# Performance work log

Hardware: AMD Instinct MI355X
Metric: run time of the kernel (lower is better)

Reference implementation:

```python
import math
import jax, jax.numpy as jnp
import numpy as np

MAX_DEGREE = 4
FOUR_PI = 4.0 * math.pi


def _assoc_legendre(ct, st, L):
    """Associated Legendre P_l^m(ct) with Condon-Shortley phase, m>=0.
    Returns dict P[(l, m)] of arrays shaped like ct."""
    P = {(0, 0): jnp.ones_like(ct)}
    # diagonal: P_m^m = (-1)^m (2m-1)!! st^m
    for m in range(1, L + 1):
        P[(m, m)] = (-(2 * m - 1)) * st * P[(m - 1, m - 1)]
    # subdiagonal: P_{m+1}^m = (2m+1) ct P_m^m
    for m in range(0, L):
        P[(m + 1, m)] = (2 * m + 1) * ct * P[(m, m)]
    # recurrence: (l-m) P_l^m = (2l-1) ct P_{l-1}^m - (l+m-1) P_{l-2}^m
    for m in range(0, L + 1):
        for l in range(m + 2, L + 1):
            P[(l, m)] = ((2 * l - 1) * ct * P[(l - 1, m)]
                         - (l + m - 1) * P[(l - 2, m)]) / (l - m)
    return P


def _sph_harm_embed(directions, L=MAX_DEGREE):
    x, y, z = directions[..., 0], directions[..., 1], directions[..., 2]
    ct = jnp.clip(z, -1.0, 1.0)                      # cos(theta)
    st = jnp.sqrt(jnp.clip(1.0 - ct * ct, 0.0, 1.0))  # sin(theta) >= 0
    phi = jnp.arctan2(y, x)
    P = _assoc_legendre(ct, st, L)
    harmonics = []
    for l in range(L + 1):
        for m in range(-l, l + 1):
            am = abs(m)
            N = math.sqrt((2 * l + 1) / FOUR_PI
                          * math.factorial(l - am) / math.factorial(l + am))
            base = N * P[(l, am)]
            re = base * jnp.cos(am * phi)
            im = base * jnp.sin(am * phi)
            if m < 0:  # Y_{l,-m} = (-1)^m conj(Y_{l,m})
                s = (-1.0) ** am
                re, im = s * re, -s * im
            harmonics.append(re)
            harmonics.append(im)
    # matches torch.stack(harmonics, dim=-1): [B, N, 2*(L+1)^2]
    return jnp.stack(harmonics, axis=-1)


def setup_inputs() -> dict:
    key = jax.random.key(0)
    d = jax.random.normal(key, (8, 262144, 3), dtype=jnp.float32)
    d = d / jnp.linalg.norm(d, axis=-1, keepdims=True)  # unit vectors
    return {"directions": d}


def reference(directions):
    return _sph_harm_embed(directions)
```

## Files before the change

kernel.cpp:

```cpp
#include <hip/hip_runtime.h>
#include <math.h>

#define WAVE 64
#define NH 50
#define HALF 32

typedef float f32x4 __attribute__((ext_vector_type(4)));

#define N00 0.28209479177387814f
#define N10 0.4886025119029199f
#define N11 0.34549414947133547f
#define N20 0.6307831305050401f
#define N21 0.2575161346821977f
#define N22 0.12875806734109884f
#define N30 0.7463526651802308f
#define N31 0.2154534560761004f
#define N32 0.06813236509610091f
#define N33 0.02781492157551894f
#define N40 0.8462843753216345f
#define N41 0.18923493915151202f
#define N42 0.04460301380579704f
#define N43 0.011920680675223072f
#define N44 0.004214597070904597f

__global__ __launch_bounds__(WAVE) void sh_embed_kernel(
    const float* __restrict__ dirs, float* __restrict__ out, int npts) {
    __shared__ float lds[HALF * NH];

    const int lane = threadIdx.x;
    const int base_pt = blockIdx.x * WAVE;
    const int pt = base_pt + lane;

    float x = 0.f, y = 0.f, z = 0.f;
    if (pt < npts) {
        const float* p = dirs + (size_t)pt * 3;
        x = p[0];
        y = p[1];
        z = p[2];
    }

    float ct = fminf(fmaxf(z, -1.f), 1.f);
    float st2 = fminf(fmaxf(1.f - ct * ct, 0.f), 1.f);
    float st = sqrtf(st2);

    float rxy2 = x * x + y * y;
    float c1, s1;
    if (rxy2 > 0.f) {
        float inv = rsqrtf(rxy2);
        c1 = x * inv;
        s1 = y * inv;
    } else {
        c1 = 1.f;
        s1 = 0.f;
    }
    float c2 = c1 * c1 - s1 * s1;
    float s2 = 2.f * c1 * s1;
    float c3 = c2 * c1 - s2 * s1;
    float s3 = s2 * c1 + c2 * s1;
    float c4 = c3 * c1 - s3 * s1;
    float s4 = s3 * c1 + c3 * s1;

    float P10 = ct;
    float P11 = -st;
    float P20 = 1.5f * ct * ct - 0.5f;
    float P21 = -3.f * ct * st;
    float P22 = 3.f * st2;
    float P30 = (5.f * ct * P20 - 2.f * P10) * (1.f / 3.f);
    float P31 = (5.f * ct * P21 - 3.f * P11) * 0.5f;
    float P32 = 15.f * ct * st2;
    float P33 = -15.f * st2 * st;
    float P40 = (7.f * ct * P30 - 3.f * P20) * 0.25f;
    float P41 = (7.f * ct * P31 - 4.f * P21) * (1.f / 3.f);
    float P42 = (7.f * ct * P32 - 5.f * P22) * 0.5f;
    float P43 = -105.f * ct * st2 * st;
    float P44 = 105.f * st2 * st2;

    float v[NH];
    v[0] = N00;
    v[1] = 0.f;
    {
        float B = N11 * P11;
        float r = B * c1, i = B * s1;
        v[2] = -r; v[3] = i;
        v[4] = N10 * P10; v[5] = 0.f;
        v[6] = r; v[7] = i;
    }
    {
        float B2 = N22 * P22, B1 = N21 * P21;
        float r2 = B2 * c2, i2 = B2 * s2;
        float r1 = B1 * c1, i1 = B1 * s1;
        v[8] = r2;  v[9] = -i2;
        v[10] = -r1; v[11] = i1;
        v[12] = N20 * P20; v[13] = 0.f;
        v[14] = r1; v[15] = i1;
        v[16] = r2; v[17] = i2;
    }
    {
        float B3 = N33 * P33, B2 = N32 * P32, B1 = N31 * P31;
        float r3 = B3 * c3, i3 = B3 * s3;
        float r2 = B2 * c2, i2 = B2 * s2;
        float r1 = B1 * c1, i1 = B1 * s1;
        v[18] = -r3; v[19] = i3;
        v[20] = r2;  v[21] = -i2;
        v[22] = -r1; v[23] = i1;
        v[24] = N30 * P30; v[25] = 0.f;
        v[26] = r1; v[27] = i1;
        v[28] = r2; v[29] = i2;
        v[30] = r3; v[31] = i3;
    }
    {
        float B4 = N44 * P44, B3 = N43 * P43, B2 = N42 * P42, B1 = N41 * P41;
        float r4 = B4 * c4, i4 = B4 * s4;
        float r3 = B3 * c3, i3 = B3 * s3;
        float r2 = B2 * c2, i2 = B2 * s2;
        float r1 = B1 * c1, i1 = B1 * s1;
        v[32] = r4;  v[33] = -i4;
        v[34] = -r3; v[35] = i3;
        v[36] = r2;  v[37] = -i2;
        v[38] = -r1; v[39] = i1;
        v[40] = N40 * P40; v[41] = 0.f;
        v[42] = r1; v[43] = i1;
        v[44] = r2; v[45] = i2;
        v[46] = r3; v[47] = i3;
        v[48] = r4; v[49] = i4;
    }

    const int valid = npts - base_pt;

    if (lane < HALF) {
        float2* row = (float2*)&lds[lane * NH];
#pragma unroll
        for (int k = 0; k < NH / 2; ++k) {
            row[k] = make_float2(v[2 * k], v[2 * k + 1]);
        }
    }
    __syncthreads();

    if (valid >= HALF) {
        const f32x4* lds4 = (const f32x4*)lds;
        f32x4* out4 = (f32x4*)(out + (size_t)base_pt * NH);
#pragma unroll
        for (int k = 0; k < 6; ++k) {
            __builtin_nontemporal_store(lds4[k * WAVE + lane], &out4[k * WAVE + lane]);
        }
        if (lane < 16) {
            __builtin_nontemporal_store(lds4[6 * WAVE + lane], &out4[6 * WAVE + lane]);
        }
    } else if (valid > 0) {
        float* outp = out + (size_t)base_pt * NH;
        int n = valid * NH;
        for (int i = lane; i < n; i += WAVE) {
            outp[i] = lds[i];
        }
    }
    __syncthreads();

    if (lane >= HALF) {
        float2* row = (float2*)&lds[(lane - HALF) * NH];
#pragma unroll
        for (int k = 0; k < NH / 2; ++k) {
            row[k] = make_float2(v[2 * k], v[2 * k + 1]);
        }
    }
    __syncthreads();

    const int valid1 = valid - HALF;
    if (valid1 >= HALF) {
        const f32x4* lds4 = (const f32x4*)lds;
        f32x4* out4 = (f32x4*)(out + (size_t)(base_pt + HALF) * NH);
#pragma unroll
        for (int k = 0; k < 6; ++k) {
            __builtin_nontemporal_store(lds4[k * WAVE + lane], &out4[k * WAVE + lane]);
        }
        if (lane < 16) {
            __builtin_nontemporal_store(lds4[6 * WAVE + lane], &out4[6 * WAVE + lane]);
        }
    } else if (valid1 > 0) {
        float* outp = out + (size_t)(base_pt + HALF) * NH;
        int n = valid1 * NH;
        for (int i = lane; i < n; i += WAVE) {
            outp[i] = lds[i];
        }
    }
}

extern "C" void kernel_launch(void* const* d_in, const int* in_sizes, int n_in,
                              void* d_out, int out_size, void* d_ws, size_t ws_size,
                              hipStream_t stream) {
    const float* dirs = (const float*)d_in[0];
    float* out = (float*)d_out;
    int npts = in_sizes[0] / 3;
    int nblocks = (npts + WAVE - 1) / WAVE;
    sh_embed_kernel<<<dim3(nblocks), dim3(WAVE), 0, stream>>>(dirs, out, npts);
}
```

Before: 427.2 us.

## Use persistent blocks looping over chunks with next-chunk input prefetch

The launch changes from one 64-thread block per 64-point chunk (32768 blocks) to a grid capped at 4096 blocks, each processing a contiguous range of chunks in a loop. Each iteration loads the next chunk's directions before computing and storing the current one, so load latency overlaps with compute and the LDS-staged stores. The aim is to cut per-block launch and scheduling overhead in this store-bound kernel. In exchange each block works serially through its chunks and an extra barrier is added per iteration, which may lower the number of stores in flight and reduce latency hiding.

```diff
diff --git a/kernel.cpp b/kernel.cpp
--- a/kernel.cpp
+++ b/kernel.cpp
@@ -4,6 +4,7 @@
 #define WAVE 64
 #define NH 50
 #define HALF 32
+#define GRID 4096
 
 typedef float f32x4 __attribute__((ext_vector_type(4)));
 
@@ -24,163 +25,182 @@
 #define N44 0.004214597070904597f
 
 __global__ __launch_bounds__(WAVE) void sh_embed_kernel(
-    const float* __restrict__ dirs, float* __restrict__ out, int npts) {
+    const float* __restrict__ dirs, float* __restrict__ out, int npts,
+    int nchunks, int cpb) {
     __shared__ float lds[HALF * NH];
 
     const int lane = threadIdx.x;
-    const int base_pt = blockIdx.x * WAVE;
-    const int pt = base_pt + lane;
+    const int c0 = blockIdx.x * cpb;
+    if (c0 >= nchunks) return;
+    const int c1 = (c0 + cpb < nchunks) ? (c0 + cpb) : nchunks;
 
     float x = 0.f, y = 0.f, z = 0.f;
-    if (pt < npts) {
-        const float* p = dirs + (size_t)pt * 3;
-        x = p[0];
-        y = p[1];
-        z = p[2];
+    {
+        int pt = c0 * WAVE + lane;
+        if (pt < npts) {
+            const float* p = dirs + (size_t)pt * 3;
+            x = p[0]; y = p[1]; z = p[2];
+        }
     }
 
-    float ct = fminf(fmaxf(z, -1.f), 1.f);
-    float st2 = fminf(fmaxf(1.f - ct * ct, 0.f), 1.f);
-    float st = sqrtf(st2);
-
-    float rxy2 = x * x + y * y;
-    float c1, s1;
-    if (rxy2 > 0.f) {
-        float inv = rsqrtf(rxy2);
-        c1 = x * inv;
-        s1 = y * inv;
-    } else {
-        c1 = 1.f;
-        s1 = 0.f;
-    }
-    float c2 = c1 * c1 - s1 * s1;
-    float s2 = 2.f * c1 * s1;
-    float c3 = c2 * c1 - s2 * s1;
-    float s3 = s2 * c1 + c2 * s1;
-    float c4 = c3 * c1 - s3 * s1;
-    float s4 = s3 * c1 + c3 * s1;
-
-    float P10 = ct;
-    float P11 = -st;
-    float P20 = 1.5f * ct * ct - 0.5f;
-    float P21 = -3.f * ct * st;
-    float P22 = 3.f * st2;
-    float P30 = (5.f * ct * P20 - 2.f * P10) * (1.f / 3.f);
-    float P31 = (5.f * ct * P21 - 3.f * P11) * 0.5f;
-    float P32 = 15.f * ct * st2;
-    float P33 = -15.f * st2 * st;
-    float P40 = (7.f * ct * P30 - 3.f * P20) * 0.25f;
-    float P41 = (7.f * ct * P31 - 4.f * P21) * (1.f / 3.f);
-    float P42 = (7.f * ct * P32 - 5.f * P22) * 0.5f;
-    float P43 = -105.f * ct * st2 * st;
-    float P44 = 105.f * st2 * st2;
-
-    float v[NH];
-    v[0] = N00;
-    v[1] = 0.f;
-    {
-        float B = N11 * P11;
-        float r = B * c1, i = B * s1;
-        v[2] = -r; v[3] = i;
-        v[4] = N10 * P10; v[5] = 0.f;
-        v[6] = r; v[7] = i;
-    }
-    {
-        float B2 = N22 * P22, B1 = N21 * P21;
-        float r2 = B2 * c2, i2 = B2 * s2;
-        float r1 = B1 * c1, i1 = B1 * s1;
-        v[8] = r2;  v[9] = -i2;
-        v[10] = -r1; v[11] = i1;
-        v[12] = N20 * P20; v[13] = 0.f;
-        v[14] = r1; v[15] = i1;
-        v[16] = r2; v[17] = i2;
-    }
-    {
-        float B3 = N33 * P33, B2 = N32 * P32, B1 = N31 * P31;
-        float r3 = B3 * c3, i3 = B3 * s3;
-        float r2 = B2 * c2, i2 = B2 * s2;
-        float r1 = B1 * c1, i1 = B1 * s1;
-        v[18] = -r3; v[19] = i3;
-        v[20] = r2;  v[21] = -i2;
-        v[22] = -r1; v[23] = i1;
-        v[24] = N30 * P30; v[25] = 0.f;
-        v[26] = r1; v[27] = i1;
-        v[28] = r2; v[29] = i2;
-        v[30] = r3; v[31] = i3;
-    }
-    {
-        float B4 = N44 * P44, B3 = N43 * P43, B2 = N42 * P42, B1 = N41 * P41;
-        float r4 = B4 * c4, i4 = B4 * s4;
-        float r3 = B3 * c3, i3 = B3 * s3;
-        float r2 = B2 * c2, i2 = B2 * s2;
-        float r1 = B1 * c1, i1 = B1 * s1;
-        v[32] = r4;  v[33] = -i4;
-        v[34] = -r3; v[35] = i3;
-        v[36] = r2;  v[37] = -i2;
-        v[38] = -r1; v[39] = i1;
-        v[40] = N40 * P40; v[41] = 0.f;
-        v[42] = r1; v[43] = i1;
-        v[44] = r2; v[45] = i2;
-        v[46] = r3; v[47] = i3;
-        v[48] = r4; v[49] = i4;
-    }
-
-    const int valid = npts - base_pt;
-
-    if (lane < HALF) {
-        float2* row = (float2*)&lds[lane * NH];
-#pragma unroll
-        for (int k = 0; k < NH / 2; ++k) {
-            row[k] = make_float2(v[2 * k], v[2 * k + 1]);
-        }
-    }
-    __syncthreads();
-
-    if (valid >= HALF) {
-        const f32x4* lds4 = (const f32x4*)lds;
-        f32x4* out4 = (f32x4*)(out + (size_t)base_pt * NH);
-#pragma unroll
-        for (int k = 0; k < 6; ++k) {
-            __builtin_nontemporal_store(lds4[k * WAVE + lane], &out4[k * WAVE + lane]);
-        }
-        if (lane < 16) {
-            __builtin_nontemporal_store(lds4[6 * WAVE + lane], &out4[6 * WAVE + lane]);
-        }
-    } else if (valid > 0) {
-        float* outp = out + (size_t)base_pt * NH;
-        int n = valid * NH;
-        for (int i = lane; i < n; i += WAVE) {
-            outp[i] = lds[i];
-        }
-    }
-    __syncthreads();
-
-    if (lane >= HALF) {
-        float2* row = (float2*)&lds[(lane - HALF) * NH];
-#pragma unroll
-        for (int k = 0; k < NH / 2; ++k) {
-            row[k] = make_float2(v[2 * k], v[2 * k + 1]);
-        }
-    }
-    __syncthreads();
-
-    const int valid1 = valid - HALF;
-    if (valid1 >= HALF) {
-        const f32x4* lds4 = (const f32x4*)lds;
-        f32x4* out4 = (f32x4*)(out + (size_t)(base_pt + HALF) * NH);
-#pragma unroll
-        for (int k = 0; k < 6; ++k) {
-            __builtin_nontemporal_store(lds4[k * WAVE + lane], &out4[k * WAVE + lane]);
-        }
-        if (lane < 16) {
-            __builtin_nontemporal_store(lds4[6 * WAVE + lane], &out4[6 * WAVE + lane]);
-        }
-    } else if (valid1 > 0) {
-        float* outp = out + (size_t)(base_pt + HALF) * NH;
-        int n = valid1 * NH;
-        for (int i = lane; i < n; i += WAVE) {
-            outp[i] = lds[i];
-        }
+    for (int c = c0; c < c1; ++c) {
+        const int base_pt = c * WAVE;
+
+        float nx = 0.f, ny = 0.f, nz = 0.f;
+        if (c + 1 < c1) {
+            int npt = (c + 1) * WAVE + lane;
+            if (npt < npts) {
+                const float* p = dirs + (size_t)npt * 3;
+                nx = p[0]; ny = p[1]; nz = p[2];
+            }
+        }
+
+        float ct = fminf(fmaxf(z, -1.f), 1.f);
+        float st2 = fminf(fmaxf(1.f - ct * ct, 0.f), 1.f);
+        float st = sqrtf(st2);
+
+        float rxy2 = x * x + y * y;
+        float c1p, s1;
+        if (rxy2 > 0.f) {
+            float inv = rsqrtf(rxy2);
+            c1p = x * inv;
+            s1 = y * inv;
+        } else {
+            c1p = 1.f;
+            s1 = 0.f;
+        }
+        float c2 = c1p * c1p - s1 * s1;
+        float s2 = 2.f * c1p * s1;
+        float c3 = c2 * c1p - s2 * s1;
+        float s3 = s2 * c1p + c2 * s1;
+        float c4 = c3 * c1p - s3 * s1;
+        float s4 = s3 * c1p + c3 * s1;
+
+        float P10 = ct;
+        float P11 = -st;
+        float P20 = 1.5f * ct * ct - 0.5f;
+        float P21 = -3.f * ct * st;
+        float P22 = 3.f * st2;
+        float P30 = (5.f * ct * P20 - 2.f * P10) * (1.f / 3.f);
+        float P31 = (5.f * ct * P21 - 3.f * P11) * 0.5f;
+        float P32 = 15.f * ct * st2;
+        float P33 = -15.f * st2 * st;
+        float P40 = (7.f * ct * P30 - 3.f * P20) * 0.25f;
+        float P41 = (7.f * ct * P31 - 4.f * P21) * (1.f / 3.f);
+        float P42 = (7.f * ct * P32 - 5.f * P22) * 0.5f;
+        float P43 = -105.f * ct * st2 * st;
+        float P44 = 105.f * st2 * st2;
+
+        float v[NH];
+        v[0] = N00;
+        v[1] = 0.f;
+        {
+            float B = N11 * P11;
+            float r = B * c1p, i = B * s1;
+            v[2] = -r; v[3] = i;
+            v[4] = N10 * P10; v[5] = 0.f;
+            v[6] = r; v[7] = i;
+        }
+        {
+            float B2 = N22 * P22, B1 = N21 * P21;
+            float r2 = B2 * c2, i2 = B2 * s2;
+            float r1 = B1 * c1p, i1 = B1 * s1;
+            v[8] = r2;  v[9] = -i2;
+            v[10] = -r1; v[11] = i1;
+            v[12] = N20 * P20; v[13] = 0.f;
+            v[14] = r1; v[15] = i1;
+            v[16] = r2; v[17] = i2;
+        }
+        {
+            float B3 = N33 * P33, B2 = N32 * P32, B1 = N31 * P31;
+            float r3 = B3 * c3, i3 = B3 * s3;
+            float r2 = B2 * c2, i2 = B2 * s2;
+            float r1 = B1 * c1p, i1 = B1 * s1;
+            v[18] = -r3; v[19] = i3;
+            v[20] = r2;  v[21] = -i2;
+            v[22] = -r1; v[23] = i1;
+            v[24] = N30 * P30; v[25] = 0.f;
+            v[26] = r1; v[27] = i1;
+            v[28] = r2; v[29] = i2;
+            v[30] = r3; v[31] = i3;
+        }
+        {
+            float B4 = N44 * P44, B3 = N43 * P43, B2 = N42 * P42, B1 = N41 * P41;
+            float r4 = B4 * c4, i4 = B4 * s4;
+            float r3 = B3 * c3, i3 = B3 * s3;
+            float r2 = B2 * c2, i2 = B2 * s2;
+            float r1 = B1 * c1p, i1 = B1 * s1;
+            v[32] = r4;  v[33] = -i4;
+            v[34] = -r3; v[35] = i3;
+            v[36] = r2;  v[37] = -i2;
+            v[38] = -r1; v[39] = i1;
+            v[40] = N40 * P40; v[41] = 0.f;
+            v[42] = r1; v[43] = i1;
+            v[44] = r2; v[45] = i2;
+            v[46] = r3; v[47] = i3;
+            v[48] = r4; v[49] = i4;
+        }
+
+        const int valid = npts - base_pt;
+
+        if (lane < HALF) {
+            float2* row = (float2*)&lds[lane * NH];
+#pragma unroll
+            for (int k = 0; k < NH / 2; ++k) {
+                row[k] = make_float2(v[2 * k], v[2 * k + 1]);
+            }
+        }
+        __syncthreads();
+
+        if (valid >= HALF) {
+            const f32x4* lds4 = (const f32x4*)lds;
+            f32x4* out4 = (f32x4*)(out + (size_t)base_pt * NH);
+#pragma unroll
+            for (int k = 0; k < 6; ++k) {
+                __builtin_nontemporal_store(lds4[k * WAVE + lane], &out4[k * WAVE + lane]);
+            }
+            if (lane < 16) {
+                __builtin_nontemporal_store(lds4[6 * WAVE + lane], &out4[6 * WAVE + lane]);
+            }
+        } else if (valid > 0) {
+            float* outp = out + (size_t)base_pt * NH;
+            int n = valid * NH;
+            for (int i = lane; i < n; i += WAVE) {
+                outp[i] = lds[i];
+            }
+        }
+        __syncthreads();
+
+        if (lane >= HALF) {
+            float2* row = (float2*)&lds[(lane - HALF) * NH];
+#pragma unroll
+            for (int k = 0; k < NH / 2; ++k) {
+                row[k] = make_float2(v[2 * k], v[2 * k + 1]);
+            }
+        }
+        __syncthreads();
+
+        const int valid1 = valid - HALF;
+        if (valid1 >= HALF) {
+            const f32x4* lds4 = (const f32x4*)lds;
+            f32x4* out4 = (f32x4*)(out + (size_t)(base_pt + HALF) * NH);
+#pragma unroll
+            for (int k = 0; k < 6; ++k) {
+                __builtin_nontemporal_store(lds4[k * WAVE + lane], &out4[k * WAVE + lane]);
+            }
+            if (lane < 16) {
+                __builtin_nontemporal_store(lds4[6 * WAVE + lane], &out4[6 * WAVE + lane]);
+            }
+        } else if (valid1 > 0) {
+            float* outp = out + (size_t)(base_pt + HALF) * NH;
+            int n = valid1 * NH;
+            for (int i = lane; i < n; i += WAVE) {
+                outp[i] = lds[i];
+            }
+        }
+        __syncthreads();
+
+        x = nx; y = ny; z = nz;
     }
 }
 
@@ -190,6 +210,8 @@
     const float* dirs = (const float*)d_in[0];
     float* out = (float*)d_out;
     int npts = in_sizes[0] / 3;
-    int nblocks = (npts + WAVE - 1) / WAVE;
-    sh_embed_kernel<<<dim3(nblocks), dim3(WAVE), 0, stream>>>(dirs, out, npts);
+    int nchunks = (npts + WAVE - 1) / WAVE;
+    int grid = (nchunks < GRID) ? nchunks : GRID;
+    int cpb = (nchunks + grid - 1) / grid;
+    sh_embed_kernel<<<dim3(grid), dim3(WAVE), 0, stream>>>(dirs, out, npts, nchunks, cpb);
 }
```

After: 435.4 us. No clear change (+1.9%).
